# Optimization experiments

Measured on AMD Instinct MI355X. Metric: run time of the kernel, lower is better.

## Reference

```python
import jax, jax.numpy as jnp
import numpy as np
import math

B, NG, LS, E = 2, 8, 512, 1024
NH = 16
HD = E // NH
EPS = 1e-6


def rms_norm(x, w):
    xf = x.astype(jnp.float32)
    n = xf * jax.lax.rsqrt(jnp.mean(xf * xf, axis=-1, keepdims=True) + EPS)
    return n.astype(x.dtype) * w


def rotate(x):
    # pairs (a,b) -> (-b, a), matching view(...,-1,2).flip(-1); x[...,0]*=-1
    x2 = x.reshape(*x.shape[:-1], HD // 2, 2)
    out = jnp.stack([-x2[..., 1], x2[..., 0]], axis=-1)
    return out.reshape(x.shape)


def setup_inputs() -> dict:
    key = jax.random.key(0)
    k1, k2, k3 = jax.random.split(key, 3)
    x = jax.random.normal(k1, (B, NG, LS, E), dtype=jnp.float32)
    W_qkv = jax.random.normal(k2, (E, 3 * E), dtype=jnp.float32) * (1.0 / math.sqrt(E))
    ln_w = jnp.ones((E,), dtype=jnp.float32)
    W_proj = jax.random.normal(k3, (E, E), dtype=jnp.float32) * (1.0 / math.sqrt(E))
    return {"x": x, "W_qkv": W_qkv, "ln_w": ln_w, "W_proj": W_proj}


def reference(x, W_qkv, ln_w, W_proj):
    b, ng, ls, _ = x.shape
    qkv = jnp.einsum('bgsc,ce->bgse', x, W_qkv)  # fused QKV projection
    q, k, v = jnp.split(qkv, 3, axis=-1)
    # QK RMSNorm over full embedding dim (before head split)
    q = rms_norm(q, ln_w)
    k = rms_norm(k, ln_w)
    # [B, ng, nh, ls, hd]
    q = q.reshape(b, ng, ls, NH, HD).swapaxes(2, 3)
    k = k.reshape(b, ng, ls, NH, HD).swapaxes(2, 3)
    v = v.reshape(b, ng, ls, NH, HD).swapaxes(2, 3)
    # RoPE (repo's variant: angles duplicated across halves, adjacent-pair rotate)
    pos = 10000.0 ** ((-2.0 * jnp.arange(0, HD, 2, dtype=jnp.float32) - 1.0) / HD)
    token_seq = jnp.arange(ls, dtype=jnp.float32)[:, None] * pos[None, :]  # [ls, hd/2]
    rot = jnp.concatenate([token_seq, token_seq], axis=-1)  # [ls, hd]
    cos, sin = jnp.cos(rot), jnp.sin(rot)
    q = q * cos + rotate(q) * sin
    k = k * cos + rotate(k) * sin
    # causal attention, scale = 1/sqrt(head_dim) (muP=False)
    scale = 1.0 / math.sqrt(HD)
    scores = jnp.einsum('bgnqd,bgnkd->bgnqk', q, k) * scale
    causal = jnp.tril(jnp.ones((ls, ls), dtype=bool))
    scores = jnp.where(causal, scores, jnp.finfo(scores.dtype).min)
    att = jax.nn.softmax(scores, axis=-1)
    y = jnp.einsum('bgnqk,bgnkd->bgnqd', att, v)
    y = y.swapaxes(2, 3).reshape(b, ng, ls, E)
    y = jnp.einsum('bgse,ef->bgsf', y, W_proj)
    return y
```

## Files before the change

### kernel.cpp

```cpp
#include <hip/hip_runtime.h>

typedef unsigned short u16;
typedef unsigned int   u32;
typedef __attribute__((ext_vector_type(8))) short bf16x8;
typedef __attribute__((ext_vector_type(4))) float f32x4;

#define MFMA16(a,b,c) __builtin_amdgcn_mfma_f32_16x16x32_bf16((a),(b),(c),0,0,0)
#define GLD16(gp, lp) __builtin_amdgcn_global_load_lds((const __attribute__((address_space(1))) u32*)(gp), (__attribute__((address_space(3))) u32*)(lp), 16, 0, 0)

#define B_   2
#define NG_  8
#define LS_  512
#define E_   1024
#define NH_  16
#define HD_  64
#define NTOK 8192

__device__ __forceinline__ u16 f2bu(float f){
  u32 u = __builtin_bit_cast(u32, f);
  u32 r = u + 0x7FFFu + ((u >> 16) & 1u);
  return (u16)(r >> 16);
}
__device__ __forceinline__ float b2f(u16 h){
  u32 u = ((u32)h) << 16;
  return __builtin_bit_cast(float, u);
}

__global__ __launch_bounds__(256) void k_conv_x(const float* __restrict__ x, u16* __restrict__ xb){
  int i = blockIdx.x * 256 + threadIdx.x;
  float4 v = ((const float4*)x)[i];
  ((ushort4*)xb)[i] = make_ushort4(f2bu(v.x), f2bu(v.y), f2bu(v.z), f2bu(v.w));
}

__global__ __launch_bounds__(256) void k_transpose(const float* __restrict__ W, u16* __restrict__ WT,
                                                   int Kd, int Nd){
  __shared__ float tile[32][33];
  int tx = threadIdx.x & 31, ty = threadIdx.x >> 5;
  int c0 = blockIdx.x * 32, r0 = blockIdx.y * 32;
  #pragma unroll
  for (int i = 0; i < 4; i++)
    tile[ty + i*8][tx] = W[(size_t)(r0 + ty + i*8) * Nd + c0 + tx];
  __syncthreads();
  #pragma unroll
  for (int i = 0; i < 4; i++)
    WT[(size_t)(c0 + ty + i*8) * Kd + r0 + tx] = f2bu(tile[tx][ty + i*8]);
}

__global__ __launch_bounds__(256) void k_rope_table(float* __restrict__ ct, float* __restrict__ st){
  int i = blockIdx.x * 256 + threadIdx.x;
  int s = i >> 6, d = i & 63, j = d & 31;
  float freq = powf(10000.f, -(4.f * (float)j + 1.f) / 64.f);
  float th = (float)s * freq;
  ct[i] = cosf(th);
  st[i] = sinf(th);
}

template <typename OutT>
__global__ __launch_bounds__(256, 2) void k_gemm_bt(const u16* __restrict__ A, const u16* __restrict__ Bt,
                                                    OutT* __restrict__ C, int M, int N, int K){
  int nbn = N >> 7;
  int cpx = gridDim.x >> 3;
  int bid = (blockIdx.x & 7) * cpx + (blockIdx.x >> 3);
  int tm = bid / nbn, tn = bid % nbn;
  int tid = threadIdx.x;
  int w = tid >> 6, l = tid & 63;
  int lr = l & 15, lg = l >> 4;
  int wm = (w >> 1) * 64, wn = (w & 1) * 64;

  __shared__ u16 smem[2][2][128 * 64];

  const u16* Ab = A  + (size_t)(tm * 128) * K;
  const u16* Bb = Bt + (size_t)(tn * 128) * K;
  int NT = K >> 6;

  int srow0 = tid >> 3, ssl = tid & 7;
  auto stage = [&](int t, int s){
    int k0 = t << 6;
    #pragma unroll
    for (int q = 0; q < 4; q++){
      int row = q * 32 + srow0;
      int sc  = (ssl ^ (row & 7)) << 3;
      GLD16(Ab + (size_t)row * K + k0 + sc, &smem[s][0][q * 2048 + tid * 8]);
    }
    #pragma unroll
    for (int q = 0; q < 4; q++){
      int row = q * 32 + srow0;
      int sc  = (ssl ^ (row & 7)) << 3;
      GLD16(Bb + (size_t)row * K + k0 + sc, &smem[s][1][q * 2048 + tid * 8]);
    }
  };

  f32x4 acc[4][4] = {};

  stage(0, 0);
  stage(1, 1);
  asm volatile("s_waitcnt vmcnt(8)" ::: "memory");
  asm volatile("s_barrier" ::: "memory");

  for (int t = 0; t < NT; t++){
    int s = t & 1;
    const u16* As = smem[s][0];
    const u16* Bs = smem[s][1];
    bf16x8 bfr[4][2], afr[2][2];
    #pragma unroll
    for (int j = 0; j < 4; j++){
      int rb = wn + j * 16 + lr;
      #pragma unroll
      for (int kk = 0; kk < 2; kk++)
        bfr[j][kk] = *(const bf16x8*)&Bs[rb * 64 + ((kk * 32 + lg * 8) ^ ((rb & 7) << 3))];
    }
    #pragma unroll
    for (int i = 0; i < 2; i++){
      int ra = wm + i * 16 + lr;
      #pragma unroll
      for (int kk = 0; kk < 2; kk++)
        afr[i][kk] = *(const bf16x8*)&As[ra * 64 + ((kk * 32 + lg * 8) ^ ((ra & 7) << 3))];
    }
    __builtin_amdgcn_s_setprio(1);
    #pragma unroll
    for (int i = 0; i < 2; i++)
      #pragma unroll
      for (int j = 0; j < 4; j++){
        acc[i][j] = MFMA16(afr[i][0], bfr[j][0], acc[i][j]);
        acc[i][j] = MFMA16(afr[i][1], bfr[j][1], acc[i][j]);
      }
    __builtin_amdgcn_s_setprio(0);
    asm volatile("s_barrier" ::: "memory");
    #pragma unroll
    for (int i = 0; i < 2; i++){
      int ra = wm + (i + 2) * 16 + lr;
      #pragma unroll
      for (int kk = 0; kk < 2; kk++)
        afr[i][kk] = *(const bf16x8*)&As[ra * 64 + ((kk * 32 + lg * 8) ^ ((ra & 7) << 3))];
    }
    __builtin_amdgcn_s_setprio(1);
    #pragma unroll
    for (int i = 0; i < 2; i++)
      #pragma unroll
      for (int j = 0; j < 4; j++){
        acc[i + 2][j] = MFMA16(afr[i][0], bfr[j][0], acc[i + 2][j]);
        acc[i + 2][j] = MFMA16(afr[i][1], bfr[j][1], acc[i + 2][j]);
      }
    __builtin_amdgcn_s_setprio(0);
    asm volatile("s_barrier" ::: "memory");
    if (t + 2 < NT){
      stage(t + 2, s);
      asm volatile("s_waitcnt vmcnt(8)" ::: "memory");
      asm volatile("s_barrier" ::: "memory");
    } else if (t + 2 == NT){
      asm volatile("s_waitcnt vmcnt(0)" ::: "memory");
      asm volatile("s_barrier" ::: "memory");
    }
  }

  #pragma unroll
  for (int i = 0; i < 4; i++)
    #pragma unroll
    for (int j = 0; j < 4; j++)
      #pragma unroll
      for (int r = 0; r < 4; r++){
        int row = tm * 128 + wm + i * 16 + lg * 4 + r;
        int col = tn * 128 + wn + j * 16 + lr;
        float v = acc[i][j][r];
        if constexpr (sizeof(OutT) == 2) C[(size_t)row * N + col] = f2bu(v);
        else                             C[(size_t)row * N + col] = v;
      }
}

__global__ __launch_bounds__(256) void k_norm_rope(const u16* __restrict__ qkv, const float* __restrict__ lnw,
                                                   const float* __restrict__ ct, const float* __restrict__ st,
                                                   u16* __restrict__ qh, u16* __restrict__ kh, u16* __restrict__ vh){
  int tok = blockIdx.x;
  int t = threadIdx.x;
  int s = tok & (LS_ - 1);
  int bg = tok >> 9;
  const u16* row = qkv + (size_t)tok * 3072;
  int e0 = t * 4;

  ushort4 q4 = *(const ushort4*)&row[e0];
  ushort4 k4 = *(const ushort4*)&row[1024 + e0];
  ushort4 v4 = *(const ushort4*)&row[2048 + e0];
  float qf[4] = {b2f(q4.x), b2f(q4.y), b2f(q4.z), b2f(q4.w)};
  float kf[4] = {b2f(k4.x), b2f(k4.y), b2f(k4.z), b2f(k4.w)};

  float qss = 0.f, kss = 0.f;
  #pragma unroll
  for (int j = 0; j < 4; j++){ qss += qf[j]*qf[j]; kss += kf[j]*kf[j]; }
  #pragma unroll
  for (int o = 32; o; o >>= 1){ qss += __shfl_down(qss, o); kss += __shfl_down(kss, o); }
  __shared__ float redq[4], redk[4];
  if ((t & 63) == 0){ redq[t >> 6] = qss; redk[t >> 6] = kss; }
  __syncthreads();
  float qsum = redq[0] + redq[1] + redq[2] + redq[3];
  float ksum = redk[0] + redk[1] + redk[2] + redk[3];
  float qr = rsqrtf(qsum * (1.f / 1024.f) + 1e-6f);
  float kr = rsqrtf(ksum * (1.f / 1024.f) + 1e-6f);

  float qn[4], kn[4];
  #pragma unroll
  for (int j = 0; j < 4; j++){
    float wv = lnw[e0 + j];
    qn[j] = qf[j] * qr * wv;
    kn[j] = kf[j] * kr * wv;
  }
  int d0 = e0 & 63, h = e0 >> 6;
  const float* cr = ct + s * 64 + d0;
  const float* sr = st + s * 64 + d0;
  float qo[4], ko[4];
  #pragma unroll
  for (int p = 0; p < 4; p += 2){
    float c0 = cr[p], s0 = sr[p], c1 = cr[p+1], s1 = sr[p+1];
    qo[p]   = qn[p]   * c0 - qn[p+1] * s0;
    qo[p+1] = qn[p+1] * c1 + qn[p]   * s1;
    ko[p]   = kn[p]   * c0 - kn[p+1] * s0;
    ko[p+1] = kn[p+1] * c1 + kn[p]   * s1;
  }
  size_t oidx = (((size_t)bg * NH_ + h) * LS_ + s) * HD_ + d0;
  *(ushort4*)&qh[oidx] = make_ushort4(f2bu(qo[0]*0.125f), f2bu(qo[1]*0.125f), f2bu(qo[2]*0.125f), f2bu(qo[3]*0.125f));
  *(ushort4*)&kh[oidx] = make_ushort4(f2bu(ko[0]), f2bu(ko[1]), f2bu(ko[2]), f2bu(ko[3]));
  *(ushort4*)&vh[oidx] = v4;
}

__global__ __launch_bounds__(256) void k_vt(const u16* __restrict__ vh, u16* __restrict__ vt){
  int head = blockIdx.x >> 3, sb = blockIdx.x & 7;
  int s0 = sb * 64;
  __shared__ u16 t[64 * 72];
  const u16* src = vh + (size_t)head * LS_ * HD_ + (size_t)s0 * HD_;
  u16* dst = vt + (size_t)head * HD_ * LS_;
  #pragma unroll
  for (int p = 0; p < 2; p++){
    int idx = p * 256 + threadIdx.x;
    int r = idx >> 3, c8 = (idx & 7) * 8;
    *(bf16x8*)&t[r * 72 + c8] = *(const bf16x8*)&src[r * HD_ + c8];
  }
  __syncthreads();
  #pragma unroll
  for (int p = 0; p < 2; p++){
    int idx = p * 256 + threadIdx.x;
    int d = idx >> 3, s8 = (idx & 7) * 8;
    u16 tmp[8];
    #pragma unroll
    for (int j = 0; j < 8; j++) tmp[j] = t[(s8 + j) * 72 + d];
    *(bf16x8*)&dst[(size_t)d * LS_ + s0 + s8] = *(bf16x8*)tmp;
  }
}

__global__ __launch_bounds__(256) void k_attn(const u16* __restrict__ qh, const u16* __restrict__ kh,
                                              const u16* __restrict__ vt, u16* __restrict__ ytok){
  int bid = blockIdx.x;
  int head = bid & 255, pb = bid >> 8;
  int tid = threadIdx.x;
  int w = tid >> 6, l = tid & 63;
  int lr = l & 15, lg = l >> 4;
  int j = (w == 0) ? pb : (w == 1) ? (15 - pb) : (w == 2) ? (pb + 4) : (11 - pb);
  int q0 = j * 32;
  int ntw = (j >> 1) + 1;

  const u16* Qp = qh + (size_t)head * LS_ * HD_;
  const u16* Kp = kh + (size_t)head * LS_ * HD_;
  const u16* Vp = vt + (size_t)head * HD_ * LS_;
  int bg = head >> 4, h = head & 15;
  u16* Yb = ytok + (size_t)bg * LS_ * E_ + h * HD_;

  bf16x8 aq[2][2];
  #pragma unroll
  for (int mi = 0; mi < 2; mi++)
    #pragma unroll
    for (int kk = 0; kk < 2; kk++)
      aq[mi][kk] = *(const bf16x8*)&Qp[(q0 + mi*16 + lr) * 64 + kk * 32 + lg * 8];

  __shared__ u16 Pl[4][32 * 72];
  u16* Pw = Pl[w];

  f32x4 o[2][4] = {};
  float mrun[2] = {-1e30f, -1e30f}, lrun[2] = {0.f, 0.f};

  for (int tkv = 0; tkv < ntw; tkv++){
    int kv0 = tkv * 64;
    f32x4 sa[2][4] = {};
    __builtin_amdgcn_s_setprio(1);
    #pragma unroll
    for (int nk = 0; nk < 4; nk++){
      bf16x8 k0 = *(const bf16x8*)&Kp[(kv0 + nk*16 + lr) * 64 + lg * 8];
      bf16x8 k1 = *(const bf16x8*)&Kp[(kv0 + nk*16 + lr) * 64 + 32 + lg * 8];
      #pragma unroll
      for (int mi = 0; mi < 2; mi++){
        sa[mi][nk] = MFMA16(k0, aq[mi][0], sa[mi][nk]);
        sa[mi][nk] = MFMA16(k1, aq[mi][1], sa[mi][nk]);
      }
    }
    __builtin_amdgcn_s_setprio(0);
    if (kv0 + 63 > q0){
      #pragma unroll
      for (int mi = 0; mi < 2; mi++){
        int qg = q0 + mi*16 + lr;
        #pragma unroll
        for (int nk = 0; nk < 4; nk++)
          #pragma unroll
          for (int r = 0; r < 4; r++){
            int kg = kv0 + nk*16 + lg*4 + r;
            if (kg > qg) sa[mi][nk][r] = -1e30f;
          }
      }
    }
    float alpha[2];
    #pragma unroll
    for (int mi = 0; mi < 2; mi++){
      float pmax = sa[mi][0][0];
      #pragma unroll
      for (int nk = 0; nk < 4; nk++)
        #pragma unroll
        for (int r = 0; r < 4; r++) pmax = fmaxf(pmax, sa[mi][nk][r]);
      pmax = fmaxf(pmax, __shfl_xor(pmax, 16));
      pmax = fmaxf(pmax, __shfl_xor(pmax, 32));

      float mnew = fmaxf(mrun[mi], pmax);
      alpha[mi] = __expf(mrun[mi] - mnew);
      mrun[mi] = mnew;

      float psum = 0.f;
      #pragma unroll
      for (int nk = 0; nk < 4; nk++)
        #pragma unroll
        for (int r = 0; r < 4; r++){
          float pv = __expf(sa[mi][nk][r] - mnew);
          sa[mi][nk][r] = pv;
          psum += pv;
        }
      psum += __shfl_xor(psum, 16);
      psum += __shfl_xor(psum, 32);
      lrun[mi] = lrun[mi] * alpha[mi] + psum;
    }
    #pragma unroll
    for (int r = 0; r < 4; r++){
      float a0 = __shfl(alpha[0], lg * 4 + r);
      float a1 = __shfl(alpha[1], lg * 4 + r);
      #pragma unroll
      for (int nd = 0; nd < 4; nd++){ o[0][nd][r] *= a0; o[1][nd][r] *= a1; }
    }
    #pragma unroll
    for (int mi = 0; mi < 2; mi++)
      #pragma unroll
      for (int nk = 0; nk < 4; nk++){
        u32 d0 = (u32)f2bu(sa[mi][nk][0]) | ((u32)f2bu(sa[mi][nk][1]) << 16);
        u32 d1 = (u32)f2bu(sa[mi][nk][2]) | ((u32)f2bu(sa[mi][nk][3]) << 16);
        *(u32*)&Pw[(mi*16 + lr) * 72 + nk * 16 + lg * 4]     = d0;
        *(u32*)&Pw[(mi*16 + lr) * 72 + nk * 16 + lg * 4 + 2] = d1;
      }
    bf16x8 pa[2][2];
    #pragma unroll
    for (int mi = 0; mi < 2; mi++){
      pa[mi][0] = *(const bf16x8*)&Pw[(mi*16 + lr) * 72 + lg * 8];
      pa[mi][1] = *(const bf16x8*)&Pw[(mi*16 + lr) * 72 + 32 + lg * 8];
    }
    __builtin_amdgcn_s_setprio(1);
    #pragma unroll
    for (int nd = 0; nd < 4; nd++){
      bf16x8 bv0 = *(const bf16x8*)&Vp[(nd*16 + lr) * 512 + kv0 + lg * 8];
      bf16x8 bv1 = *(const bf16x8*)&Vp[(nd*16 + lr) * 512 + kv0 + 32 + lg * 8];
      #pragma unroll
      for (int mi = 0; mi < 2; mi++){
        o[mi][nd] = MFMA16(pa[mi][0], bv0, o[mi][nd]);
        o[mi][nd] = MFMA16(pa[mi][1], bv1, o[mi][nd]);
      }
    }
    __builtin_amdgcn_s_setprio(0);
  }

  #pragma unroll
  for (int mi = 0; mi < 2; mi++){
    float linv = 1.f / lrun[mi];
    #pragma unroll
    for (int r = 0; r < 4; r++){
      float ir = __shfl(linv, lg * 4 + r);
      int qg = q0 + mi*16 + lg * 4 + r;
      #pragma unroll
      for (int nd = 0; nd < 4; nd++)
        Yb[(size_t)qg * E_ + nd * 16 + lr] = f2bu(o[mi][nd][r] * ir);
    }
  }
}

extern "C" void kernel_launch(void* const* d_in, const int* in_sizes, int n_in,
                              void* d_out, int out_size, void* d_ws, size_t ws_size,
                              hipStream_t stream){
  const float* x     = (const float*)d_in[0];
  const float* Wqkv  = (const float*)d_in[1];
  const float* lnw   = (const float*)d_in[2];
  const float* Wproj = (const float*)d_in[3];
  float* out = (float*)d_out;

  u16* p = (u16*)d_ws;
  u16* xb     = p; p += (size_t)NTOK * E_;
  u16* wqkvT  = p; p += (size_t)3 * E_ * E_;
  u16* wprojT = p; p += (size_t)E_ * E_;
  u16* qkv    = p; p += (size_t)NTOK * 3 * E_;
  u16* qhp    = p; p += (size_t)NTOK * E_;
  u16* khp    = p; p += (size_t)NTOK * E_;
  u16* vhp    = p; p += (size_t)NTOK * E_;
  float* ct = (float*)p;
  float* st = ct + LS_ * HD_;
  u16* vtp = qkv;

  k_conv_x<<<8192, 256, 0, stream>>>(x, xb);
  k_transpose<<<dim3(96, 32), 256, 0, stream>>>(Wqkv, wqkvT, 1024, 3072);
  k_transpose<<<dim3(32, 32), 256, 0, stream>>>(Wproj, wprojT, 1024, 1024);
  k_rope_table<<<128, 256, 0, stream>>>(ct, st);
  k_gemm_bt<u16><<<64 * 24, 256, 0, stream>>>(xb, wqkvT, qkv, NTOK, 3 * E_, E_);
  k_norm_rope<<<NTOK, 256, 0, stream>>>(qkv, lnw, ct, st, qhp, khp, vhp);
  k_vt<<<2048, 256, 0, stream>>>(vhp, vtp);
  k_attn<<<1024, 256, 0, stream>>>(qhp, khp, vtp, xb);
  k_gemm_bt<float><<<64 * 8, 256, 0, stream>>>(xb, wprojT, out, NTOK, E_, E_);
}
```

Measured before the change: 182.4 us.

## Split attention into single-wave blocks, prefetch K/V, lazily rescale softmax

The attention kernel moves from 256-thread blocks holding four query tiles each to one 64-thread block per 32-row query tile, with blocks ordered so the longest causal rows launch first. K for the next tile is prefetched into registers and V is loaded before the softmax, so global loads overlap with compute. Rescaling of the running max and output is skipped unless the max grows by more than 8, and bf16 packing uses the hardware cvt_pk instruction. The cost is more registers per wave, more and smaller blocks, and a small numerical risk from the lazy max update.

After: 166.6 us. -8.7%, faster.

```diff
diff --git a/kernel.cpp b/kernel.cpp
--- a/kernel.cpp
+++ b/kernel.cpp
@@ -24,6 +24,9 @@
 __device__ __forceinline__ float b2f(u16 h){
   u32 u = ((u32)h) << 16;
   return __builtin_bit_cast(float, u);
+}
+__device__ __forceinline__ u32 pk2(float lo, float hi){
+  u32 r; asm("v_cvt_pk_bf16_f32 %0, %1, %2" : "=v"(r) : "v"(lo), "v"(hi)); return r;
 }
 
 __global__ __launch_bounds__(256) void k_conv_x(const float* __restrict__ x, u16* __restrict__ xb){
@@ -245,14 +248,13 @@
   }
 }
 
-__global__ __launch_bounds__(256) void k_attn(const u16* __restrict__ qh, const u16* __restrict__ kh,
-                                              const u16* __restrict__ vt, u16* __restrict__ ytok){
+__global__ __launch_bounds__(64) void k_attn(const u16* __restrict__ qh, const u16* __restrict__ kh,
+                                             const u16* __restrict__ vt, u16* __restrict__ ytok){
   int bid = blockIdx.x;
-  int head = bid & 255, pb = bid >> 8;
-  int tid = threadIdx.x;
-  int w = tid >> 6, l = tid & 63;
+  int head = bid & 255;
+  int j = 15 - (bid >> 8);
+  int l = threadIdx.x & 63;
   int lr = l & 15, lg = l >> 4;
-  int j = (w == 0) ? pb : (w == 1) ? (15 - pb) : (w == 2) ? (pb + 4) : (11 - pb);
   int q0 = j * 32;
   int ntw = (j >> 1) + 1;
 
@@ -269,27 +271,40 @@
     for (int kk = 0; kk < 2; kk++)
       aq[mi][kk] = *(const bf16x8*)&Qp[(q0 + mi*16 + lr) * 64 + kk * 32 + lg * 8];
 
-  __shared__ u16 Pl[4][32 * 72];
-  u16* Pw = Pl[w];
+  __shared__ u16 Pw[32 * 72];
 
   f32x4 o[2][4] = {};
   float mrun[2] = {-1e30f, -1e30f}, lrun[2] = {0.f, 0.f};
+
+  bf16x8 kr[4][2];
+  auto loadK = [&](int kv0){
+    #pragma unroll
+    for (int nk = 0; nk < 4; nk++){
+      kr[nk][0] = *(const bf16x8*)&Kp[(kv0 + nk*16 + lr) * 64 + lg * 8];
+      kr[nk][1] = *(const bf16x8*)&Kp[(kv0 + nk*16 + lr) * 64 + 32 + lg * 8];
+    }
+  };
+  loadK(0);
 
   for (int tkv = 0; tkv < ntw; tkv++){
     int kv0 = tkv * 64;
     f32x4 sa[2][4] = {};
     __builtin_amdgcn_s_setprio(1);
     #pragma unroll
-    for (int nk = 0; nk < 4; nk++){
-      bf16x8 k0 = *(const bf16x8*)&Kp[(kv0 + nk*16 + lr) * 64 + lg * 8];
-      bf16x8 k1 = *(const bf16x8*)&Kp[(kv0 + nk*16 + lr) * 64 + 32 + lg * 8];
+    for (int nk = 0; nk < 4; nk++)
       #pragma unroll
       for (int mi = 0; mi < 2; mi++){
-        sa[mi][nk] = MFMA16(k0, aq[mi][0], sa[mi][nk]);
-        sa[mi][nk] = MFMA16(k1, aq[mi][1], sa[mi][nk]);
-      }
-    }
+        sa[mi][nk] = MFMA16(kr[nk][0], aq[mi][0], sa[mi][nk]);
+        sa[mi][nk] = MFMA16(kr[nk][1], aq[mi][1], sa[mi][nk]);
+      }
     __builtin_amdgcn_s_setprio(0);
+    if (tkv + 1 < ntw) loadK(kv0 + 64);
+    bf16x8 vr[4][2];
+    #pragma unroll
+    for (int nd = 0; nd < 4; nd++){
+      vr[nd][0] = *(const bf16x8*)&Vp[(nd*16 + lr) * 512 + kv0 + lg * 8];
+      vr[nd][1] = *(const bf16x8*)&Vp[(nd*16 + lr) * 512 + kv0 + 32 + lg * 8];
+    }
     if (kv0 + 63 > q0){
       #pragma unroll
       for (int mi = 0; mi < 2; mi++){
@@ -303,49 +318,57 @@
           }
       }
     }
-    float alpha[2];
+    float pmax[2];
     #pragma unroll
     for (int mi = 0; mi < 2; mi++){
-      float pmax = sa[mi][0][0];
+      float pm = sa[mi][0][0];
       #pragma unroll
       for (int nk = 0; nk < 4; nk++)
         #pragma unroll
-        for (int r = 0; r < 4; r++) pmax = fmaxf(pmax, sa[mi][nk][r]);
-      pmax = fmaxf(pmax, __shfl_xor(pmax, 16));
-      pmax = fmaxf(pmax, __shfl_xor(pmax, 32));
-
-      float mnew = fmaxf(mrun[mi], pmax);
-      alpha[mi] = __expf(mrun[mi] - mnew);
-      mrun[mi] = mnew;
-
+        for (int r = 0; r < 4; r++) pm = fmaxf(pm, sa[mi][nk][r]);
+      pm = fmaxf(pm, __shfl_xor(pm, 16));
+      pm = fmaxf(pm, __shfl_xor(pm, 32));
+      pmax[mi] = pm;
+    }
+    float dm = fmaxf(pmax[0] - mrun[0], pmax[1] - mrun[1]);
+    if (!__all(dm <= 8.f)){
+      float alpha[2];
+      #pragma unroll
+      for (int mi = 0; mi < 2; mi++){
+        float mnew = fmaxf(mrun[mi], pmax[mi]);
+        alpha[mi] = __expf(mrun[mi] - mnew);
+        mrun[mi] = mnew;
+        lrun[mi] *= alpha[mi];
+      }
+      #pragma unroll
+      for (int r = 0; r < 4; r++){
+        float a0 = __shfl(alpha[0], lg * 4 + r);
+        float a1 = __shfl(alpha[1], lg * 4 + r);
+        #pragma unroll
+        for (int nd = 0; nd < 4; nd++){ o[0][nd][r] *= a0; o[1][nd][r] *= a1; }
+      }
+    }
+    #pragma unroll
+    for (int mi = 0; mi < 2; mi++){
       float psum = 0.f;
       #pragma unroll
       for (int nk = 0; nk < 4; nk++)
         #pragma unroll
         for (int r = 0; r < 4; r++){
-          float pv = __expf(sa[mi][nk][r] - mnew);
+          float pv = __expf(sa[mi][nk][r] - mrun[mi]);
           sa[mi][nk][r] = pv;
           psum += pv;
         }
       psum += __shfl_xor(psum, 16);
       psum += __shfl_xor(psum, 32);
-      lrun[mi] = lrun[mi] * alpha[mi] + psum;
-    }
-    #pragma unroll
-    for (int r = 0; r < 4; r++){
-      float a0 = __shfl(alpha[0], lg * 4 + r);
-      float a1 = __shfl(alpha[1], lg * 4 + r);
-      #pragma unroll
-      for (int nd = 0; nd < 4; nd++){ o[0][nd][r] *= a0; o[1][nd][r] *= a1; }
+      lrun[mi] += psum;
     }
     #pragma unroll
     for (int mi = 0; mi < 2; mi++)
       #pragma unroll
       for (int nk = 0; nk < 4; nk++){
-        u32 d0 = (u32)f2bu(sa[mi][nk][0]) | ((u32)f2bu(sa[mi][nk][1]) << 16);
-        u32 d1 = (u32)f2bu(sa[mi][nk][2]) | ((u32)f2bu(sa[mi][nk][3]) << 16);
-        *(u32*)&Pw[(mi*16 + lr) * 72 + nk * 16 + lg * 4]     = d0;
-        *(u32*)&Pw[(mi*16 + lr) * 72 + nk * 16 + lg * 4 + 2] = d1;
+        *(u32*)&Pw[(mi*16 + lr) * 72 + nk * 16 + lg * 4]     = pk2(sa[mi][nk][0], sa[mi][nk][1]);
+        *(u32*)&Pw[(mi*16 + lr) * 72 + nk * 16 + lg * 4 + 2] = pk2(sa[mi][nk][2], sa[mi][nk][3]);
       }
     bf16x8 pa[2][2];
     #pragma unroll
@@ -355,15 +378,12 @@
     }
     __builtin_amdgcn_s_setprio(1);
     #pragma unroll
-    for (int nd = 0; nd < 4; nd++){
-      bf16x8 bv0 = *(const bf16x8*)&Vp[(nd*16 + lr) * 512 + kv0 + lg * 8];
-      bf16x8 bv1 = *(const bf16x8*)&Vp[(nd*16 + lr) * 512 + kv0 + 32 + lg * 8];
+    for (int nd = 0; nd < 4; nd++)
       #pragma unroll
       for (int mi = 0; mi < 2; mi++){
-        o[mi][nd] = MFMA16(pa[mi][0], bv0, o[mi][nd]);
-        o[mi][nd] = MFMA16(pa[mi][1], bv1, o[mi][nd]);
-      }
-    }
+        o[mi][nd] = MFMA16(pa[mi][0], vr[nd][0], o[mi][nd]);
+        o[mi][nd] = MFMA16(pa[mi][1], vr[nd][1], o[mi][nd]);
+      }
     __builtin_amdgcn_s_setprio(0);
   }
 
@@ -409,6 +429,6 @@
   k_gemm_bt<u16><<<64 * 24, 256, 0, stream>>>(xb, wqkvT, qkv, NTOK, 3 * E_, E_);
   k_norm_rope<<<NTOK, 256, 0, stream>>>(qkv, lnw, ct, st, qhp, khp, vhp);
   k_vt<<<2048, 256, 0, stream>>>(vhp, vtp);
-  k_attn<<<1024, 256, 0, stream>>>(qhp, khp, vtp, xb);
+  k_attn<<<4096, 64, 0, stream>>>(qhp, khp, vtp, xb);
   k_gemm_bt<float><<<64 * 8, 256, 0, stream>>>(xb, wprojT, out, NTOK, E_, E_);
 }
```
